# Kernel optimization log

Hardware: AMD Instinct MI355X
Metric: run time of the kernel (lower is better)

The kernel has to match this reference:

```python
import jax, jax.numpy as jnp
import numpy as np

N = 50000      # nodes
E = 800000     # edges (avg degree 16)
F = 128        # num_features
H = 128        # hidden_channels
C = 16         # num_classes
KEEP = 0.5     # dropout keep prob


def setup_inputs() -> dict:
    key = jax.random.key(0)
    ks = jax.random.split(key, 7)
    x = jax.random.normal(ks[0], (N, F), dtype=jnp.float32)
    edge_index = jax.random.randint(ks[1], (2, E), 0, N, dtype=jnp.int64)
    W1 = jax.random.normal(ks[2], (F, H), dtype=jnp.float32) / np.float32(np.sqrt(F))
    b1 = jnp.zeros((H,), dtype=jnp.float32)
    W2 = jax.random.normal(ks[3], (H, C), dtype=jnp.float32) / np.float32(np.sqrt(H))
    b2 = jnp.zeros((C,), dtype=jnp.float32)
    # deterministic dropout mask (train-mode dropout, prob=0.5), pre-scaled by 1/keep
    dropout_mask = (jax.random.uniform(ks[4], (N, H)) < KEEP).astype(jnp.float32) / np.float32(KEEP)
    return {"x": x, "edge_index": edge_index, "W1": W1, "b1": b1,
            "W2": W2, "b2": b2, "dropout_mask": dropout_mask}


def _gather_mean(h, src, dst, n_nodes):
    # irregular gather (h[src]) + segment scatter-add at dst, then mean by in-degree
    agg = jax.ops.segment_sum(h[src], dst, num_segments=n_nodes)  # [N, c]
    deg = jax.ops.segment_sum(jnp.ones_like(dst, dtype=h.dtype), dst, num_segments=n_nodes)
    return agg / jnp.maximum(deg, 1.0)[:, None]


def reference(x, edge_index, W1, b1, W2, b2, dropout_mask):
    src, dst = edge_index[0], edge_index[1]
    # linmaps1: 0th->1st order broadcast; identity for singleton reference domains
    h = _gather_mean(x, src, dst, N)          # ConvolutionalLayer_1P #1: gather
    h = h @ W1 + b1                           # linear transform
    h = jax.nn.relu(h)
    h = h * dropout_mask                      # Dropout(prob=0.5)
    h = _gather_mean(h, src, dst, N)          # ConvolutionalLayer_1P #2: gather
    out = h @ W2 + b2
    # linmaps0: 1st->0th order reduce; identity for singleton domains
    return out
```

## Files before the change

kernel.cpp:

```cpp
#include <hip/hip_runtime.h>

#define NNODES 50000
#define NEDGES 800000
#define FDIM 128
#define HDIM 128
#define CDIM 16

#define NBUCK 256
#define BCAP 6144
#define NBA 391
#define NMB 782

typedef __attribute__((ext_vector_type(8))) short bf16x8;
typedef __attribute__((ext_vector_type(4))) float f32x4;

__device__ __forceinline__ ushort f32_to_bf16_rne(float f) {
  unsigned u = __float_as_uint(f);
  unsigned rounded = u + 0x7fffu + ((u >> 16) & 1u);
  return (ushort)(rounded >> 16);
}
__device__ __forceinline__ float bf_lo(unsigned u) { return __uint_as_float(u << 16); }
__device__ __forceinline__ float bf_hi(unsigned u) { return __uint_as_float(u & 0xffff0000u); }

__global__ __launch_bounds__(256) void k_binA(
    const int* __restrict__ src, const int* __restrict__ dst,
    int* __restrict__ gcur, unsigned* __restrict__ ebuf,
    const float* __restrict__ mask, unsigned* __restrict__ maskb) {
  __shared__ int cnt[NBUCK];
  __shared__ int base[NBUCK];
  int tid = threadIdx.x;
  if (blockIdx.x < NBA) {
    int e0 = blockIdx.x * 2048;
    cnt[tid] = 0;
    __syncthreads();
    int sv[8], dv[8];
    #pragma unroll
    for (int i = 0; i < 8; ++i) {
      int e = e0 + i * 256 + tid;
      if (e < NEDGES) {
        sv[i] = src[e];
        dv[i] = dst[e];
        atomicAdd(&cnt[dv[i] >> 8], 1);
      } else {
        dv[i] = -1;
      }
    }
    __syncthreads();
    base[tid] = atomicAdd(&gcur[tid], cnt[tid]);
    cnt[tid] = 0;
    __syncthreads();
    #pragma unroll
    for (int i = 0; i < 8; ++i) {
      if (dv[i] >= 0) {
        int b = dv[i] >> 8;
        int pos = base[b] + atomicAdd(&cnt[b], 1);
        if (pos < BCAP)
          ebuf[b * BCAP + pos] = ((unsigned)(dv[i] & 255) << 16) | (unsigned)sv[i];
      }
    }
    return;
  }
  int t = (blockIdx.x - NBA) * 256 + tid;
  if (t < 200000) {
    const float* mp = mask + (size_t)t * 32;
    unsigned bits = 0;
    #pragma unroll
    for (int i = 0; i < 8; ++i) {
      float4 m = *reinterpret_cast<const float4*>(mp + i * 4);
      bits |= (m.x != 0.f ? 1u : 0u) << (i * 4 + 0);
      bits |= (m.y != 0.f ? 1u : 0u) << (i * 4 + 1);
      bits |= (m.z != 0.f ? 1u : 0u) << (i * 4 + 2);
      bits |= (m.w != 0.f ? 1u : 0u) << (i * 4 + 3);
    }
    maskb[t] = bits;
  }
}

__global__ __launch_bounds__(256) void k_binB_cast(
    const int* __restrict__ gcur, const unsigned* __restrict__ ebuf,
    int* __restrict__ deg, int* __restrict__ offs, ushort* __restrict__ ssrc,
    const float* __restrict__ x, ushort* __restrict__ xh,
    const float* __restrict__ W1, ushort* __restrict__ W1T,
    const float* __restrict__ W2, ushort* __restrict__ W2T) {
  __shared__ int s[NBUCK];
  __shared__ int doff[NBUCK];
  __shared__ int dcur[NBUCK];
  int tid = threadIdx.x;
  if (blockIdx.x < NBUCK) {
    int b = blockIdx.x;
    int c = gcur[tid];
    if (c > BCAP) c = BCAP;
    s[tid] = c;
    for (int off = 1; off < 256; off <<= 1) {
      __syncthreads();
      int t = (tid >= off) ? s[tid - off] : 0;
      __syncthreads();
      s[tid] += t;
    }
    __syncthreads();
    int my_base = (b > 0) ? s[b - 1] : 0;
    int count = s[b] - my_base;

    dcur[tid] = 0;
    __syncthreads();
    const unsigned* eb = &ebuf[b * BCAP];
    for (int e = tid; e < count; e += 256) {
      atomicAdd(&dcur[eb[e] >> 16], 1);
    }
    __syncthreads();
    int dn = dcur[tid];
    s[tid] = dn;
    for (int off = 1; off < 256; off <<= 1) {
      __syncthreads();
      int t = (tid >= off) ? s[tid - off] : 0;
      __syncthreads();
      s[tid] += t;
    }
    __syncthreads();
    doff[tid] = s[tid] - dn;
    int node = b * 256 + tid;
    if (node < NNODES) {
      deg[node] = dn;
      offs[node] = my_base + doff[tid];
    }
    dcur[tid] = 0;
    __syncthreads();

    for (int e = tid; e < count; e += 256) {
      unsigned v = eb[e];
      int loc = v >> 16;
      int pos = my_base + doff[loc] + atomicAdd(&dcur[loc], 1);
      ssrc[pos] = (ushort)(v & 0xffffu);
    }
    return;
  }
  int t = (blockIdx.x - NBUCK) * 256 + tid;
  if (t < 1600000) {
    float4 v = *reinterpret_cast<const float4*>(&x[t * 4]);
    ushort4 o;
    o.x = f32_to_bf16_rne(v.x);
    o.y = f32_to_bf16_rne(v.y);
    o.z = f32_to_bf16_rne(v.z);
    o.w = f32_to_bf16_rne(v.w);
    *reinterpret_cast<ushort4*>(&xh[t * 4]) = o;
    return;
  }
  t -= 1600000;
  if (t < 16384) {
    int c = t >> 7, k = t & 127;
    W1T[c * 128 + k] = f32_to_bf16_rne(W1[k * 128 + c]);
    return;
  }
  t -= 16384;
  if (t < 2048) {
    int c = t >> 7, k = t & 127;
    W2T[c * 128 + k] = f32_to_bf16_rne(W2[k * 16 + c]);
  }
}

#define HT_STRIDE 132
__global__ __launch_bounds__(256) void k_fused1(
    const ushort* __restrict__ xh, const int* __restrict__ offs,
    const int* __restrict__ deg, const ushort* __restrict__ ssrc,
    const ushort* __restrict__ W1T, const float* __restrict__ b1,
    const unsigned* __restrict__ maskb, const ushort* __restrict__ W2T,
    ushort* __restrict__ zh) {
  __shared__ ushort sh[16 * HT_STRIDE];
  __shared__ ushort ht[16 * HT_STRIDE];
  int tid = threadIdx.x;
  int grp = tid >> 4;
  int l16 = tid & 15;
  int nw = blockIdx.x * 16;
  int n = nw + grp;
  int start = offs[n];
  int d = deg[n];
  const ushort* base = xh + l16 * 8;
  float a0[8] = {0,0,0,0,0,0,0,0};
  float a1[8] = {0,0,0,0,0,0,0,0};
  float a2[8] = {0,0,0,0,0,0,0,0};
  float a3[8] = {0,0,0,0,0,0,0,0};
  int j = 0;
  for (; j + 3 < d; j += 4) {
    int s0 = ssrc[start + j + 0];
    int s1 = ssrc[start + j + 1];
    int s2 = ssrc[start + j + 2];
    int s3 = ssrc[start + j + 3];
    uint4 u0 = *reinterpret_cast<const uint4*>(base + s0 * FDIM);
    uint4 u1 = *reinterpret_cast<const uint4*>(base + s1 * FDIM);
    uint4 u2 = *reinterpret_cast<const uint4*>(base + s2 * FDIM);
    uint4 u3 = *reinterpret_cast<const uint4*>(base + s3 * FDIM);
    a0[0] += bf_lo(u0.x); a0[1] += bf_hi(u0.x); a0[2] += bf_lo(u0.y); a0[3] += bf_hi(u0.y);
    a0[4] += bf_lo(u0.z); a0[5] += bf_hi(u0.z); a0[6] += bf_lo(u0.w); a0[7] += bf_hi(u0.w);
    a1[0] += bf_lo(u1.x); a1[1] += bf_hi(u1.x); a1[2] += bf_lo(u1.y); a1[3] += bf_hi(u1.y);
    a1[4] += bf_lo(u1.z); a1[5] += bf_hi(u1.z); a1[6] += bf_lo(u1.w); a1[7] += bf_hi(u1.w);
    a2[0] += bf_lo(u2.x); a2[1] += bf_hi(u2.x); a2[2] += bf_lo(u2.y); a2[3] += bf_hi(u2.y);
    a2[4] += bf_lo(u2.z); a2[5] += bf_hi(u2.z); a2[6] += bf_lo(u2.w); a2[7] += bf_hi(u2.w);
    a3[0] += bf_lo(u3.x); a3[1] += bf_hi(u3.x); a3[2] += bf_lo(u3.y); a3[3] += bf_hi(u3.y);
    a3[4] += bf_lo(u3.z); a3[5] += bf_hi(u3.z); a3[6] += bf_lo(u3.w); a3[7] += bf_hi(u3.w);
  }
  for (; j < d; ++j) {
    int s0 = ssrc[start + j];
    uint4 u0 = *reinterpret_cast<const uint4*>(base + s0 * FDIM);
    a0[0] += bf_lo(u0.x); a0[1] += bf_hi(u0.x); a0[2] += bf_lo(u0.y); a0[3] += bf_hi(u0.y);
    a0[4] += bf_lo(u0.z); a0[5] += bf_hi(u0.z); a0[6] += bf_lo(u0.w); a0[7] += bf_hi(u0.w);
  }
  float inv = 1.0f / (float)(d > 0 ? d : 1);
  unsigned r[4];
  #pragma unroll
  for (int k = 0; k < 4; ++k) {
    float e0 = (a0[2 * k] + a1[2 * k] + a2[2 * k] + a3[2 * k]) * inv;
    float e1 = (a0[2 * k + 1] + a1[2 * k + 1] + a2[2 * k + 1] + a3[2 * k + 1]) * inv;
    r[k] = (unsigned)f32_to_bf16_rne(e0) | ((unsigned)f32_to_bf16_rne(e1) << 16);
  }
  *reinterpret_cast<uint4*>(&sh[grp * HT_STRIDE + l16 * 8]) =
      (uint4){r[0], r[1], r[2], r[3]};
  __syncthreads();

  int w = tid >> 6;
  int lane = tid & 63;
  int m = lane & 15, quad = lane >> 4;
  int ct0 = 2 * w, ct1 = 2 * w + 1;

  bf16x8 af[4];
  #pragma unroll
  for (int kk = 0; kk < 4; ++kk) {
    const ushort* ap = &sh[m * HT_STRIDE + kk * 32 + quad * 8];
    ushort4 alo = *reinterpret_cast<const ushort4*>(ap);
    ushort4 ahi = *reinterpret_cast<const ushort4*>(ap + 4);
    af[kk] = (bf16x8){(short)alo.x, (short)alo.y, (short)alo.z, (short)alo.w,
                      (short)ahi.x, (short)ahi.y, (short)ahi.z, (short)ahi.w};
  }
  f32x4 acc0 = (f32x4){0.f, 0.f, 0.f, 0.f};
  f32x4 acc1 = (f32x4){0.f, 0.f, 0.f, 0.f};
  const ushort* bp0 = &W1T[(size_t)(ct0 * 16 + m) * 128 + quad * 8];
  const ushort* bp1 = &W1T[(size_t)(ct1 * 16 + m) * 128 + quad * 8];
  #pragma unroll
  for (int kk = 0; kk < 4; ++kk) {
    acc0 = __builtin_amdgcn_mfma_f32_16x16x32_bf16(
        af[kk], *reinterpret_cast<const bf16x8*>(bp0 + kk * 32), acc0, 0, 0, 0);
    acc1 = __builtin_amdgcn_mfma_f32_16x16x32_bf16(
        af[kk], *reinterpret_cast<const bf16x8*>(bp1 + kk * 32), acc1, 0, 0, 0);
  }

  unsigned mbw[4];
  #pragma unroll
  for (int rr = 0; rr < 4; ++rr) {
    mbw[rr] = maskb[(size_t)(nw + quad * 4 + rr) * 4 + w];
  }
  float bb0 = b1[ct0 * 16 + m];
  float bb1 = b1[ct1 * 16 + m];
  int sh0 = m;
  int sh1 = 16 + m;
  #pragma unroll
  for (int rr = 0; rr < 4; ++rr) {
    float v0 = acc0[rr] + bb0;
    v0 = v0 > 0.f ? v0 : 0.f;
    v0 = ((mbw[rr] >> sh0) & 1u) ? (v0 + v0) : 0.f;
    ht[(quad * 4 + rr) * HT_STRIDE + ct0 * 16 + m] = f32_to_bf16_rne(v0);
    float v1 = acc1[rr] + bb1;
    v1 = v1 > 0.f ? v1 : 0.f;
    v1 = ((mbw[rr] >> sh1) & 1u) ? (v1 + v1) : 0.f;
    ht[(quad * 4 + rr) * HT_STRIDE + ct1 * 16 + m] = f32_to_bf16_rne(v1);
  }
  __syncthreads();

  if (w == 0) {
    f32x4 zacc = (f32x4){0.f, 0.f, 0.f, 0.f};
    #pragma unroll
    for (int kk = 0; kk < 4; ++kk) {
      const ushort* ap = &ht[m * HT_STRIDE + kk * 32 + quad * 8];
      ushort4 alo = *reinterpret_cast<const ushort4*>(ap);
      ushort4 ahi = *reinterpret_cast<const ushort4*>(ap + 4);
      bf16x8 afr = (bf16x8){(short)alo.x, (short)alo.y, (short)alo.z, (short)alo.w,
                            (short)ahi.x, (short)ahi.y, (short)ahi.z, (short)ahi.w};
      bf16x8 b2f = *reinterpret_cast<const bf16x8*>(&W2T[m * 128 + kk * 32 + quad * 8]);
      zacc = __builtin_amdgcn_mfma_f32_16x16x32_bf16(afr, b2f, zacc, 0, 0, 0);
    }
    #pragma unroll
    for (int rr = 0; rr < 4; ++rr) {
      zh[(size_t)(nw + quad * 4 + rr) * 16 + m] = f32_to_bf16_rne(zacc[rr]);
    }
  }
}

__global__ __launch_bounds__(256) void k_spmm2(
    const ushort* __restrict__ zh, const int* __restrict__ offs,
    const int* __restrict__ deg, const ushort* __restrict__ ssrc,
    const float* __restrict__ b2, float* __restrict__ out) {
  int tid = threadIdx.x;
  int nl = tid >> 3, c2 = tid & 7;
  int n = blockIdx.x * 32 + nl;
  if (n >= NNODES) return;
  int start = offs[n], d = deg[n];
  const ushort* zb = zh + c2 * 2;
  float a0 = 0.f, a1 = 0.f, b0 = 0.f, b1v = 0.f;
  float c0 = 0.f, c1 = 0.f, d0 = 0.f, d1 = 0.f;
  int j = 0;
  for (; j + 7 < d; j += 8) {
    int s0 = ssrc[start + j + 0], s1 = ssrc[start + j + 1];
    int s2 = ssrc[start + j + 2], s3 = ssrc[start + j + 3];
    int s4 = ssrc[start + j + 4], s5 = ssrc[start + j + 5];
    int s6 = ssrc[start + j + 6], s7 = ssrc[start + j + 7];
    unsigned u0 = *reinterpret_cast<const unsigned*>(zb + s0 * 16);
    unsigned u1 = *reinterpret_cast<const unsigned*>(zb + s1 * 16);
    unsigned u2 = *reinterpret_cast<const unsigned*>(zb + s2 * 16);
    unsigned u3 = *reinterpret_cast<const unsigned*>(zb + s3 * 16);
    unsigned u4 = *reinterpret_cast<const unsigned*>(zb + s4 * 16);
    unsigned u5 = *reinterpret_cast<const unsigned*>(zb + s5 * 16);
    unsigned u6 = *reinterpret_cast<const unsigned*>(zb + s6 * 16);
    unsigned u7 = *reinterpret_cast<const unsigned*>(zb + s7 * 16);
    a0 += bf_lo(u0); a1 += bf_hi(u0);
    b0 += bf_lo(u1); b1v += bf_hi(u1);
    c0 += bf_lo(u2); c1 += bf_hi(u2);
    d0 += bf_lo(u3); d1 += bf_hi(u3);
    a0 += bf_lo(u4); a1 += bf_hi(u4);
    b0 += bf_lo(u5); b1v += bf_hi(u5);
    c0 += bf_lo(u6); c1 += bf_hi(u6);
    d0 += bf_lo(u7); d1 += bf_hi(u7);
  }
  for (; j < d; ++j) {
    int s0 = ssrc[start + j];
    unsigned u0 = *reinterpret_cast<const unsigned*>(zb + s0 * 16);
    a0 += bf_lo(u0); a1 += bf_hi(u0);
  }
  float inv = 1.0f / (float)(d > 0 ? d : 1);
  float o0 = ((a0 + b0) + (c0 + d0)) * inv + b2[c2 * 2 + 0];
  float o1 = ((a1 + b1v) + (c1 + d1)) * inv + b2[c2 * 2 + 1];
  float2 o; o.x = o0; o.y = o1;
  *reinterpret_cast<float2*>(&out[(size_t)n * 16 + c2 * 2]) = o;
}


extern "C" void kernel_launch(void* const* d_in, const int* in_sizes, int n_in,
                              void* d_out, int out_size, void* d_ws, size_t ws_size,
                              hipStream_t stream) {
  const float* x    = (const float*)d_in[0];
  const int*   ei   = (const int*)d_in[1];
  const float* W1   = (const float*)d_in[2];
  const float* b1   = (const float*)d_in[3];
  const float* W2   = (const float*)d_in[4];
  const float* b2   = (const float*)d_in[5];
  const float* mask = (const float*)d_in[6];
  float* out = (float*)d_out;

  const int* src = ei;
  const int* dst = ei + NEDGES;

  char* ws = (char*)d_ws;
  size_t o = 0;
  auto alloc = [&](size_t bytes) -> void* {
    void* p = ws + o;
    o += (bytes + 255) & ~(size_t)255;
    return p;
  };
  ushort*   xh    = (ushort*)alloc((size_t)NNODES * 128 * 2);
  ushort*   zh    = (ushort*)alloc((size_t)NNODES * 16 * 2);
  ushort*   W1T   = (ushort*)alloc((size_t)128 * 128 * 2);
  ushort*   W2T   = (ushort*)alloc((size_t)16 * 128 * 2);
  int*      deg   = (int*)alloc((size_t)NNODES * 4);
  int*      offs  = (int*)alloc((size_t)NNODES * 4);
  int*      gcur  = (int*)alloc((size_t)NBUCK * 4);
  unsigned* ebuf  = (unsigned*)alloc((size_t)NBUCK * BCAP * 4);
  ushort*   ssrc  = (ushort*)alloc((size_t)NEDGES * 2);
  unsigned* maskb = (unsigned*)alloc((size_t)NNODES * 4 * 4);

  int cast_blocks = (1600000 + 16384 + 2048 + 255) / 256;

  hipMemsetAsync(gcur, 0, NBUCK * sizeof(int), stream);
  k_binA<<<NBA + NMB, 256, 0, stream>>>(src, dst, gcur, ebuf, mask, maskb);
  k_binB_cast<<<NBUCK + cast_blocks, 256, 0, stream>>>(gcur, ebuf, deg, offs, ssrc,
                                                       x, xh, W1, W1T, W2, W2T);
  k_fused1<<<NNODES / 16, 256, 0, stream>>>(xh, offs, deg, ssrc,
                                            W1T, b1, maskb, W2T, zh);
  k_spmm2<<<(NNODES + 31) / 32, 256, 0, stream>>>(zh, offs, deg, ssrc, b2, out);
}
```

Before: 172.2 us.

## Replace bucketed CSR build with global atomic degree count, scan, and placement

Replaces the two-pass bucket binning CSR construction with a global-atomic degree histogram, a single-block prefix scan, and an atomic-cursor placement of source indices. This drops the intermediate bucket buffer and its capacity limit, and widens the x cast to 8 elements per thread. In exchange it adds a serial single-block scan kernel, an extra launch, and contended global atomics. Edge order within each node becomes nondeterministic.

After: 348.8 us. 2.03x slower.

```diff
diff --git a/kernel.cpp b/kernel.cpp
--- a/kernel.cpp
+++ b/kernel.cpp
@@ -6,11 +6,6 @@
 #define HDIM 128
 #define CDIM 16
 
-#define NBUCK 256
-#define BCAP 6144
-#define NBA 391
-#define NMB 782
-
 typedef __attribute__((ext_vector_type(8))) short bf16x8;
 typedef __attribute__((ext_vector_type(4))) float f32x4;
 
@@ -22,45 +17,23 @@
 __device__ __forceinline__ float bf_lo(unsigned u) { return __uint_as_float(u << 16); }
 __device__ __forceinline__ float bf_hi(unsigned u) { return __uint_as_float(u & 0xffff0000u); }
 
-__global__ __launch_bounds__(256) void k_binA(
-    const int* __restrict__ src, const int* __restrict__ dst,
-    int* __restrict__ gcur, unsigned* __restrict__ ebuf,
-    const float* __restrict__ mask, unsigned* __restrict__ maskb) {
-  __shared__ int cnt[NBUCK];
-  __shared__ int base[NBUCK];
-  int tid = threadIdx.x;
-  if (blockIdx.x < NBA) {
-    int e0 = blockIdx.x * 2048;
-    cnt[tid] = 0;
-    __syncthreads();
-    int sv[8], dv[8];
-    #pragma unroll
-    for (int i = 0; i < 8; ++i) {
-      int e = e0 + i * 256 + tid;
-      if (e < NEDGES) {
-        sv[i] = src[e];
-        dv[i] = dst[e];
-        atomicAdd(&cnt[dv[i] >> 8], 1);
-      } else {
-        dv[i] = -1;
-      }
-    }
-    __syncthreads();
-    base[tid] = atomicAdd(&gcur[tid], cnt[tid]);
-    cnt[tid] = 0;
-    __syncthreads();
-    #pragma unroll
-    for (int i = 0; i < 8; ++i) {
-      if (dv[i] >= 0) {
-        int b = dv[i] >> 8;
-        int pos = base[b] + atomicAdd(&cnt[b], 1);
-        if (pos < BCAP)
-          ebuf[b * BCAP + pos] = ((unsigned)(dv[i] & 255) << 16) | (unsigned)sv[i];
-      }
-    }
+#define PRE_UNITS (200000 + 200000 + 800000 + 16384 + 2048)
+__global__ __launch_bounds__(256) void k_pre(
+    const int* __restrict__ dst, int* __restrict__ deg,
+    const float* __restrict__ mask, unsigned* __restrict__ maskb,
+    const float* __restrict__ x, ushort* __restrict__ xh,
+    const float* __restrict__ W1, ushort* __restrict__ W1T,
+    const float* __restrict__ W2, ushort* __restrict__ W2T) {
+  int t = blockIdx.x * 256 + threadIdx.x;
+  if (t < 200000) {
+    uint4 d4 = *reinterpret_cast<const uint4*>(&dst[t * 4]);
+    atomicAdd(&deg[d4.x], 1);
+    atomicAdd(&deg[d4.y], 1);
+    atomicAdd(&deg[d4.z], 1);
+    atomicAdd(&deg[d4.w], 1);
     return;
   }
-  int t = (blockIdx.x - NBA) * 256 + tid;
+  t -= 200000;
   if (t < 200000) {
     const float* mp = mask + (size_t)t * 32;
     unsigned bits = 0;
@@ -73,79 +46,21 @@
       bits |= (m.w != 0.f ? 1u : 0u) << (i * 4 + 3);
     }
     maskb[t] = bits;
-  }
-}
-
-__global__ __launch_bounds__(256) void k_binB_cast(
-    const int* __restrict__ gcur, const unsigned* __restrict__ ebuf,
-    int* __restrict__ deg, int* __restrict__ offs, ushort* __restrict__ ssrc,
-    const float* __restrict__ x, ushort* __restrict__ xh,
-    const float* __restrict__ W1, ushort* __restrict__ W1T,
-    const float* __restrict__ W2, ushort* __restrict__ W2T) {
-  __shared__ int s[NBUCK];
-  __shared__ int doff[NBUCK];
-  __shared__ int dcur[NBUCK];
-  int tid = threadIdx.x;
-  if (blockIdx.x < NBUCK) {
-    int b = blockIdx.x;
-    int c = gcur[tid];
-    if (c > BCAP) c = BCAP;
-    s[tid] = c;
-    for (int off = 1; off < 256; off <<= 1) {
-      __syncthreads();
-      int t = (tid >= off) ? s[tid - off] : 0;
-      __syncthreads();
-      s[tid] += t;
-    }
-    __syncthreads();
-    int my_base = (b > 0) ? s[b - 1] : 0;
-    int count = s[b] - my_base;
-
-    dcur[tid] = 0;
-    __syncthreads();
-    const unsigned* eb = &ebuf[b * BCAP];
-    for (int e = tid; e < count; e += 256) {
-      atomicAdd(&dcur[eb[e] >> 16], 1);
-    }
-    __syncthreads();
-    int dn = dcur[tid];
-    s[tid] = dn;
-    for (int off = 1; off < 256; off <<= 1) {
-      __syncthreads();
-      int t = (tid >= off) ? s[tid - off] : 0;
-      __syncthreads();
-      s[tid] += t;
-    }
-    __syncthreads();
-    doff[tid] = s[tid] - dn;
-    int node = b * 256 + tid;
-    if (node < NNODES) {
-      deg[node] = dn;
-      offs[node] = my_base + doff[tid];
-    }
-    dcur[tid] = 0;
-    __syncthreads();
-
-    for (int e = tid; e < count; e += 256) {
-      unsigned v = eb[e];
-      int loc = v >> 16;
-      int pos = my_base + doff[loc] + atomicAdd(&dcur[loc], 1);
-      ssrc[pos] = (ushort)(v & 0xffffu);
-    }
     return;
   }
-  int t = (blockIdx.x - NBUCK) * 256 + tid;
-  if (t < 1600000) {
-    float4 v = *reinterpret_cast<const float4*>(&x[t * 4]);
-    ushort4 o;
-    o.x = f32_to_bf16_rne(v.x);
-    o.y = f32_to_bf16_rne(v.y);
-    o.z = f32_to_bf16_rne(v.z);
-    o.w = f32_to_bf16_rne(v.w);
-    *reinterpret_cast<ushort4*>(&xh[t * 4]) = o;
+  t -= 200000;
+  if (t < 800000) {
+    float4 a = *reinterpret_cast<const float4*>(&x[(size_t)t * 8]);
+    float4 b = *reinterpret_cast<const float4*>(&x[(size_t)t * 8 + 4]);
+    uint4 o;
+    o.x = (unsigned)f32_to_bf16_rne(a.x) | ((unsigned)f32_to_bf16_rne(a.y) << 16);
+    o.y = (unsigned)f32_to_bf16_rne(a.z) | ((unsigned)f32_to_bf16_rne(a.w) << 16);
+    o.z = (unsigned)f32_to_bf16_rne(b.x) | ((unsigned)f32_to_bf16_rne(b.y) << 16);
+    o.w = (unsigned)f32_to_bf16_rne(b.z) | ((unsigned)f32_to_bf16_rne(b.w) << 16);
+    *reinterpret_cast<uint4*>(&xh[(size_t)t * 8]) = o;
     return;
   }
-  t -= 1600000;
+  t -= 800000;
   if (t < 16384) {
     int c = t >> 7, k = t & 127;
     W1T[c * 128 + k] = f32_to_bf16_rne(W1[k * 128 + c]);
@@ -156,6 +71,54 @@
     int c = t >> 7, k = t & 127;
     W2T[c * 128 + k] = f32_to_bf16_rne(W2[k * 16 + c]);
   }
+}
+
+__global__ __launch_bounds__(1024) void k_scan(
+    const int* __restrict__ deg, int* __restrict__ offs, int* __restrict__ curs) {
+  __shared__ int ps[1024];
+  int t = threadIdx.x;
+  int base = t * 49;
+  int sum = 0;
+  #pragma unroll 7
+  for (int i = 0; i < 49; ++i) {
+    int idx = base + i;
+    if (idx < NNODES) sum += deg[idx];
+  }
+  ps[t] = sum;
+  for (int off = 1; off < 1024; off <<= 1) {
+    __syncthreads();
+    int v = (t >= off) ? ps[t - off] : 0;
+    __syncthreads();
+    ps[t] += v;
+  }
+  __syncthreads();
+  int run = ps[t] - sum;
+  #pragma unroll 7
+  for (int i = 0; i < 49; ++i) {
+    int idx = base + i;
+    if (idx < NNODES) {
+      offs[idx] = run;
+      curs[idx] = run;
+      run += deg[idx];
+    }
+  }
+}
+
+__global__ __launch_bounds__(256) void k_place(
+    const int* __restrict__ src, const int* __restrict__ dst,
+    int* __restrict__ curs, ushort* __restrict__ ssrc) {
+  int t = blockIdx.x * 256 + threadIdx.x;
+  if (t >= 200000) return;
+  uint4 s4 = *reinterpret_cast<const uint4*>(&src[t * 4]);
+  uint4 d4 = *reinterpret_cast<const uint4*>(&dst[t * 4]);
+  int p0 = atomicAdd(&curs[d4.x], 1);
+  ssrc[p0] = (ushort)s4.x;
+  int p1 = atomicAdd(&curs[d4.y], 1);
+  ssrc[p1] = (ushort)s4.y;
+  int p2 = atomicAdd(&curs[d4.z], 1);
+  ssrc[p2] = (ushort)s4.z;
+  int p3 = atomicAdd(&curs[d4.w], 1);
+  ssrc[p3] = (ushort)s4.w;
 }
 
 #define HT_STRIDE 132
@@ -359,17 +322,17 @@
   ushort*   W2T   = (ushort*)alloc((size_t)16 * 128 * 2);
   int*      deg   = (int*)alloc((size_t)NNODES * 4);
   int*      offs  = (int*)alloc((size_t)NNODES * 4);
-  int*      gcur  = (int*)alloc((size_t)NBUCK * 4);
-  unsigned* ebuf  = (unsigned*)alloc((size_t)NBUCK * BCAP * 4);
+  int*      curs  = (int*)alloc((size_t)NNODES * 4);
   ushort*   ssrc  = (ushort*)alloc((size_t)NEDGES * 2);
   unsigned* maskb = (unsigned*)alloc((size_t)NNODES * 4 * 4);
 
-  int cast_blocks = (1600000 + 16384 + 2048 + 255) / 256;
-
-  hipMemsetAsync(gcur, 0, NBUCK * sizeof(int), stream);
-  k_binA<<<NBA + NMB, 256, 0, stream>>>(src, dst, gcur, ebuf, mask, maskb);
-  k_binB_cast<<<NBUCK + cast_blocks, 256, 0, stream>>>(gcur, ebuf, deg, offs, ssrc,
-                                                       x, xh, W1, W1T, W2, W2T);
+  int pre_blocks = (PRE_UNITS + 255) / 256;
+
+  hipMemsetAsync(deg, 0, (size_t)NNODES * 4, stream);
+  k_pre<<<pre_blocks, 256, 0, stream>>>(dst, deg, mask, maskb,
+                                        x, xh, W1, W1T, W2, W2T);
+  k_scan<<<1, 1024, 0, stream>>>(deg, offs, curs);
+  k_place<<<(200000 + 255) / 256, 256, 0, stream>>>(src, dst, curs, ssrc);
   k_fused1<<<NNODES / 16, 256, 0, stream>>>(xh, offs, deg, ssrc,
                                             W1T, b1, maskb, W2T, zh);
   k_spmm2<<<(NNODES + 31) / 32, 256, 0, stream>>>(zh, offs, deg, ssrc, b2, out);
```
